# Performance work log

Hardware: AMD Instinct MI355X
Metric: run time of the kernel (lower is better)

The kernel has to match this reference:

```python
import jax, jax.numpy as jnp
import numpy as np

N = 100000
E = 1600000
IN_DIM = 128
OUT_DIM = 128
H = 4
HD = OUT_DIM // H  # 32
NEG_SLOPE = 0.2
EPS_SOFTMAX = 1e-8
EPS_LN = 1e-5


def setup_inputs() -> dict:
    key = jax.random.key(0)
    ks = jax.random.split(key, 6)
    h = jax.random.normal(ks[0], (N, IN_DIM), dtype=jnp.float32)
    edge_index = jax.random.randint(ks[1], (2, E), 0, N, dtype=jnp.int32)
    W = jax.random.normal(ks[2], (IN_DIM, OUT_DIM), dtype=jnp.float32) / np.sqrt(IN_DIM)
    W_self = jax.random.normal(ks[3], (IN_DIM, OUT_DIM), dtype=jnp.float32) / np.sqrt(IN_DIM)
    a_in = jax.random.normal(ks[4], (H, 2 * HD), dtype=jnp.float32) * 0.01
    a_out = jax.random.normal(ks[5], (H, 2 * HD), dtype=jnp.float32) * 0.01
    bias = jnp.zeros((OUT_DIM,), dtype=jnp.float32)
    ln_gamma = jnp.ones((OUT_DIM,), dtype=jnp.float32)
    ln_beta = jnp.zeros((OUT_DIM,), dtype=jnp.float32)
    return {"h": h, "edge_index": edge_index, "W": W, "W_self": W_self,
            "a_in": a_in, "a_out": a_out, "bias": bias,
            "ln_gamma": ln_gamma, "ln_beta": ln_beta}


def _attention_aggregate(h_proj, sender, receiver, attn_vec, num_nodes):
    # h_proj: (N, H, HD); sender/receiver: (E,); attn_vec: (H, 2*HD)
    h_sender = h_proj[sender]      # (E, H, HD)
    h_receiver = h_proj[receiver]  # (E, H, HD)
    # e = sum over concat([h_sender, h_receiver]) * attn_vec, split halves
    e = (jnp.einsum('ehd,hd->eh', h_sender, attn_vec[:, :HD])
         + jnp.einsum('ehd,hd->eh', h_receiver, attn_vec[:, HD:]))
    e = jax.nn.leaky_relu(e, NEG_SLOPE)
    e_max = jax.ops.segment_max(e, receiver, num_segments=num_nodes)  # (N, H)
    alpha = jnp.exp(e - e_max[receiver])
    alpha_sum = jax.ops.segment_sum(alpha, receiver, num_segments=num_nodes)
    alpha = alpha / (alpha_sum[receiver] + EPS_SOFTMAX)
    msg = h_sender * alpha[..., None]  # (E, H, HD)
    return jax.ops.segment_sum(msg, receiver, num_segments=num_nodes)  # (N, H, HD)


def reference(h, edge_index, W, W_self, a_in, a_out, bias, ln_gamma, ln_beta):
    n = h.shape[0]
    h_proj = (h @ W).reshape(n, H, HD)
    h_self = h @ W_self
    src, dst = edge_index[0], edge_index[1]
    h_in = _attention_aggregate(h_proj, src, dst, a_in, n)   # 'in' direction
    h_out = _attention_aggregate(h_proj, dst, src, a_out, n)  # 'out' direction
    combined = h_self + h_in.reshape(n, -1) + h_out.reshape(n, -1) + bias
    mean = combined.mean(axis=-1, keepdims=True)
    var = combined.var(axis=-1, keepdims=True)
    normed = (combined - mean) * jax.lax.rsqrt(var + EPS_LN)
    return normed * ln_gamma + ln_beta
```

## Files before the change

kernel.cpp:

```cpp
#include <hip/hip_runtime.h>
#include <math.h>

#define HEADS 4
#define HD 32
#define DIM 128
#define NEG_SLOPE 0.2f
#define EPS_SM 1e-8f
#define EPS_LN 1e-5f
#define GROWS 64
#define SH1 9
#define PB 128

typedef _Float16 h2_t __attribute__((ext_vector_type(2)));

__device__ __forceinline__ float lrelu(float x) { return x > 0.f ? x : NEG_SLOPE * x; }
__device__ __forceinline__ unsigned pkh(float a, float b) {
    return __builtin_bit_cast(unsigned, __builtin_amdgcn_cvt_pkrtz(a, b));
}
__device__ __forceinline__ float dot2(unsigned a, unsigned b, float c) {
    return __builtin_amdgcn_fdot2(__builtin_bit_cast(h2_t, a), __builtin_bit_cast(h2_t, b), c, false);
}

template<int LIM> __device__ __forceinline__ void rmax4(float& a, float& b, float& c, float& d) {
#pragma unroll
    for (int s = 1; s < LIM; s <<= 1) {
        a = fmaxf(a, __shfl_xor(a, s, 64));
        b = fmaxf(b, __shfl_xor(b, s, 64));
        c = fmaxf(c, __shfl_xor(c, s, 64));
        d = fmaxf(d, __shfl_xor(d, s, 64));
    }
}
template<int LIM> __device__ __forceinline__ void rsum4(float& a, float& b, float& c, float& d) {
#pragma unroll
    for (int s = 1; s < LIM; s <<= 1) {
        a += __shfl_xor(a, s, 64);
        b += __shfl_xor(b, s, 64);
        c += __shfl_xor(c, s, 64);
        d += __shfl_xor(d, s, 64);
    }
}

__global__ __launch_bounds__(256) void dual_gemm_k(const float* __restrict__ h,
                                                   const float* __restrict__ W,
                                                   const float* __restrict__ V,
                                                   const float* __restrict__ a_in,
                                                   const float* __restrict__ a_out,
                                                   float* __restrict__ h_self,
                                                   unsigned* __restrict__ hp_pk,
                                                   float* __restrict__ pA0, float* __restrict__ pA1,
                                                   float* __restrict__ pB0, float* __restrict__ pB1,
                                                   int N) {
    __shared__ float As[32][GROWS];
    __shared__ float Ws[32][DIM];
    __shared__ float Vs[32][DIM];
    __shared__ float ainL[256], aoutL[256];
    const int tid = threadIdx.x;
    const int cg = tid & 15;
    const int rg = tid >> 4;
    const int row0 = blockIdx.x * GROWS;

    ainL[tid] = a_in[tid];
    aoutL[tid] = a_out[tid];

    float accP[4][8], accS[4][8];
#pragma unroll
    for (int r = 0; r < 4; ++r)
#pragma unroll
        for (int c = 0; c < 8; ++c) { accP[r][c] = 0.f; accS[r][c] = 0.f; }

    for (int kc = 0; kc < 4; ++kc) {
        __syncthreads();
#pragma unroll
        for (int p = 0; p < 2; ++p) {
            int f = tid + p * 256;
            int r = f >> 3, c4 = f & 7;
            float4 v = make_float4(0.f, 0.f, 0.f, 0.f);
            if (row0 + r < N) v = ((const float4*)h)[(size_t)(row0 + r) * 32 + kc * 8 + c4];
            As[c4 * 4 + 0][r] = v.x;
            As[c4 * 4 + 1][r] = v.y;
            As[c4 * 4 + 2][r] = v.z;
            As[c4 * 4 + 3][r] = v.w;
        }
#pragma unroll
        for (int p = 0; p < 4; ++p) {
            int f = tid + p * 256;
            int lk = f >> 5, c4 = f & 31;
            ((float4*)&Ws[lk][0])[c4] = ((const float4*)W)[(size_t)(kc * 32 + lk) * 32 + c4];
            ((float4*)&Vs[lk][0])[c4] = ((const float4*)V)[(size_t)(kc * 32 + lk) * 32 + c4];
        }
        __syncthreads();
#pragma unroll
        for (int kk = 0; kk < 32; ++kk) {
            float4 a = *(const float4*)&As[kk][rg * 4];
            float4 w0 = *(const float4*)&Ws[kk][cg * 8];
            float4 w1 = *(const float4*)&Ws[kk][cg * 8 + 4];
            float4 v0 = *(const float4*)&Vs[kk][cg * 8];
            float4 v1 = *(const float4*)&Vs[kk][cg * 8 + 4];
            float av[4] = {a.x, a.y, a.z, a.w};
            float wv[8] = {w0.x, w0.y, w0.z, w0.w, w1.x, w1.y, w1.z, w1.w};
            float vv[8] = {v0.x, v0.y, v0.z, v0.w, v1.x, v1.y, v1.z, v1.w};
#pragma unroll
            for (int r = 0; r < 4; ++r)
#pragma unroll
                for (int c = 0; c < 8; ++c) {
                    accP[r][c] += av[r] * wv[c];
                    accS[r][c] += av[r] * vv[c];
                }
        }
    }

#pragma unroll
    for (int r = 0; r < 4; ++r) {
        int row = row0 + rg * 4 + r;
        if (row < N) {
            float4 s0 = make_float4(accS[r][0], accS[r][1], accS[r][2], accS[r][3]);
            float4 s1 = make_float4(accS[r][4], accS[r][5], accS[r][6], accS[r][7]);
            ((float4*)h_self)[(size_t)row * 32 + cg * 2] = s0;
            ((float4*)h_self)[(size_t)row * 32 + cg * 2 + 1] = s1;
        }
    }

    const int head = cg >> 2, qi = cg & 3;
#pragma unroll
    for (int r = 0; r < 4; ++r) {
        float d0 = 0.f, d1 = 0.f, d2 = 0.f, d3 = 0.f;
#pragma unroll
        for (int c = 0; c < 8; ++c) {
            float v = accP[r][c];
            int k = head * 64 + qi * 8 + c;
            d0 += v * ainL[k];
            d1 += v * ainL[k + 32];
            d2 += v * aoutL[k];
            d3 += v * aoutL[k + 32];
        }
        d0 += __shfl_xor(d0, 1, 64); d0 += __shfl_xor(d0, 2, 64);
        d1 += __shfl_xor(d1, 1, 64); d1 += __shfl_xor(d1, 2, 64);
        d2 += __shfl_xor(d2, 1, 64); d2 += __shfl_xor(d2, 2, 64);
        d3 += __shfl_xor(d3, 1, 64); d3 += __shfl_xor(d3, 2, 64);
        if (qi == 0) {
            int row = row0 + rg * 4 + r;
            if (row < N) {
                pA0[row * 4 + head] = d0;
                pA1[row * 4 + head] = d1;
                pB0[row * 4 + head] = d2;
                pB1[row * 4 + head] = d3;
            }
        }
    }

#pragma unroll
    for (int r = 0; r < 4; ++r) {
        int row = row0 + rg * 4 + r;
        if (row < N) {
            uint4 pk;
            pk.x = pkh(accP[r][0], accP[r][1]);
            pk.y = pkh(accP[r][2], accP[r][3]);
            pk.z = pkh(accP[r][4], accP[r][5]);
            pk.w = pkh(accP[r][6], accP[r][7]);
            ((uint4*)hp_pk)[(size_t)row * 16 + cg] = pk;
        }
    }
}

__global__ __launch_bounds__(256) void part1a_k(const int* __restrict__ ei, int* __restrict__ cntmat,
                                                int E, int N, int NBIN) {
    __shared__ int lcnt[512];
    const int t = threadIdx.x;
    const int CH = (E + gridDim.x - 1) / gridDim.x;
    const int e0 = blockIdx.x * CH;
    const int e1 = min(e0 + CH, E);
    for (int i = t; i < 512; i += 256) lcnt[i] = 0;
    __syncthreads();
    for (int e = e0 + t; e < e1; e += 256) {
        int s = ei[e], d = ei[E + e];
        atomicAdd(&lcnt[d >> SH1], 1);
        atomicAdd(&lcnt[(N + s) >> SH1], 1);
    }
    __syncthreads();
    for (int i = t; i < NBIN; i += 256) cntmat[i * PB + blockIdx.x] = lcnt[i];
}

__global__ __launch_bounds__(128) void scanB_k(const int* __restrict__ cntmat,
                                               int* __restrict__ blkoff, int* __restrict__ btot) {
    __shared__ int ls[PB];
    const int bin = blockIdx.x;
    const int t = threadIdx.x;
    int v = cntmat[bin * PB + t];
    ls[t] = v;
    __syncthreads();
#pragma unroll
    for (int d = 1; d < PB; d <<= 1) {
        int u = (t >= d) ? ls[t - d] : 0;
        __syncthreads();
        ls[t] += u;
        __syncthreads();
    }
    blkoff[bin * PB + t] = ls[t] - v;
    if (t == PB - 1) btot[bin] = ls[t];
}

__global__ __launch_bounds__(256) void scanC_k(const int* __restrict__ btot,
                                               int* __restrict__ bbase, int NBIN, int twoE) {
    __shared__ int ls[256];
    int t = threadIdx.x;
    int i0 = 2 * t, i1 = 2 * t + 1;
    int v0 = (i0 < NBIN) ? btot[i0] : 0;
    int v1 = (i1 < NBIN) ? btot[i1] : 0;
    int pair = v0 + v1;
    ls[t] = pair;
    __syncthreads();
#pragma unroll
    for (int d = 1; d < 256; d <<= 1) {
        int u = (t >= d) ? ls[t - d] : 0;
        __syncthreads();
        ls[t] += u;
        __syncthreads();
    }
    int excl = ls[t] - pair;
    if (i0 < NBIN) bbase[i0] = excl;
    if (i1 < NBIN) bbase[i1] = excl + v0;
    if (t == 0) bbase[NBIN] = twoE;
}

__global__ __launch_bounds__(256) void part1b_k(const int* __restrict__ ei,
                                                const int* __restrict__ bbase,
                                                const int* __restrict__ blkoff,
                                                unsigned* __restrict__ rec, int E, int N, int NBIN) {
    __shared__ int gb[512];
    __shared__ int lcur[512];
    const int t = threadIdx.x;
    const int CH = (E + gridDim.x - 1) / gridDim.x;
    const int e0 = blockIdx.x * CH;
    const int e1 = min(e0 + CH, E);
    for (int i = t; i < 512; i += 256) lcur[i] = 0;
    for (int i = t; i < NBIN; i += 256) gb[i] = bbase[i] + blkoff[i * PB + blockIdx.x];
    __syncthreads();
    for (int e = e0 + t; e < e1; e += 256) {
        int s = ei[e], d = ei[E + e];
        int b1 = d >> SH1;
        int r1 = atomicAdd(&lcur[b1], 1);
        rec[gb[b1] + r1] = (unsigned)s | ((unsigned)(d & 511) << 20);
        int so = N + s;
        int b2 = so >> SH1;
        int r2 = atomicAdd(&lcur[b2], 1);
        rec[gb[b2] + r2] = (unsigned)d | ((unsigned)(so & 511) << 20);
    }
}

__global__ __launch_bounds__(256) void build2_k(const unsigned* __restrict__ rec,
                                                const int* __restrict__ bbase,
                                                int* __restrict__ off, int* __restrict__ csr,
                                                int M, int twoE, int NBIN) {
    __shared__ int lcnt[512];
    __shared__ int lcur[512];
    __shared__ int ls[256];
    const int b = blockIdx.x;
    const int t = threadIdx.x;
    const int base = bbase[b];
    const int cnt = bbase[b + 1] - base;
    const int seg0 = b << SH1;
    for (int i = t; i < 512; i += 256) lcnt[i] = 0;
    __syncthreads();
    for (int k = t; k < cnt; k += 256) atomicAdd(&lcnt[rec[base + k] >> 20], 1);
    __syncthreads();
    int v0 = lcnt[2 * t], v1 = lcnt[2 * t + 1];
    int pair = v0 + v1;
    ls[t] = pair;
    __syncthreads();
#pragma unroll
    for (int d = 1; d < 256; d <<= 1) {
        int u = (t >= d) ? ls[t - d] : 0;
        __syncthreads();
        ls[t] += u;
        __syncthreads();
    }
    int excl = ls[t] - pair;
    lcur[2 * t] = excl;
    lcur[2 * t + 1] = excl + v0;
    int sg = seg0 + 2 * t;
    if (sg < M) off[sg] = base + excl;
    if (sg + 1 < M) off[sg + 1] = base + excl + v0;
    if (b == NBIN - 1 && t == 0) off[M] = twoE;
    __syncthreads();
    for (int k = t; k < cnt; k += 256) {
        unsigned r = rec[base + k];
        int pos = atomicAdd(&lcur[r >> 20], 1);
        csr[base + pos] = (int)(r & 0xFFFFFu);
    }
}

__global__ __launch_bounds__(256) void node_aggr_ln_k(const unsigned* __restrict__ hp_pk,
                                                      const float* __restrict__ h_self,
                                                      const float* __restrict__ pA0, const float* __restrict__ pA1,
                                                      const float* __restrict__ pB0, const float* __restrict__ pB1,
                                                      const int* __restrict__ off, const int* __restrict__ csr,
                                                      const float* __restrict__ bias,
                                                      const float* __restrict__ gamma,
                                                      const float* __restrict__ beta,
                                                      float* __restrict__ out, int N) {
    __shared__ int sds[4][64];
    __shared__ uint2 wts[4][64];
    const int wave = threadIdx.x >> 6;
    const int lane = threadIdx.x & 63;
    const int n = blockIdx.x * 4 + wave;
    if (n >= N) return;
    const int l15 = lane & 15;
    const int q = lane >> 4;
    const unsigned wsel = (l15 & 4) ? 0x07060302u : 0x05040100u;
    const bool hlo = (l15 < 8);
    int* sdw = sds[wave];
    uint2* wtw = wts[wave];
    const char* hpb = (const char*)hp_pk;
    const unsigned rowoff = (unsigned)l15 << 4;

    float acc[8];
#pragma unroll
    for (int k = 0; k < 8; ++k) acc[k] = 0.f;

#pragma unroll
    for (int dir = 0; dir < 2; ++dir) {
        const int seg = (dir == 0) ? n : N + n;
        const int beg = off[seg], end = off[seg + 1];
        const int len = end - beg;
        if (len == 0) continue;
        const float* __restrict__ p0 = (dir == 0) ? pA0 : pB0;
        const float* __restrict__ p1 = (dir == 0) ? pA1 : pB1;
        float4 r1 = ((const float4*)p1)[n];

        if (len <= 64) {
            int sid = 0;
            float e0 = -INFINITY, e1 = -INFINITY, e2 = -INFINITY, e3 = -INFINITY;
            if (lane < len) {
                sid = csr[beg + lane];
                float4 r0 = ((const float4*)p0)[sid];
                e0 = lrelu(r0.x + r1.x);
                e1 = lrelu(r0.y + r1.y);
                e2 = lrelu(r0.z + r1.z);
                e3 = lrelu(r0.w + r1.w);
            }
            float m0 = e0, m1 = e1, m2 = e2, m3 = e3;
            if (len <= 16)      rmax4<16>(m0, m1, m2, m3);
            else if (len <= 32) rmax4<32>(m0, m1, m2, m3);
            else                rmax4<64>(m0, m1, m2, m3);
            float w0 = 0.f, w1 = 0.f, w2 = 0.f, w3 = 0.f;
            if (lane < len) {
                w0 = __expf(e0 - m0); w1 = __expf(e1 - m1);
                w2 = __expf(e2 - m2); w3 = __expf(e3 - m3);
            }
            float s0 = w0, s1 = w1, s2 = w2, s3 = w3;
            if (len <= 16)      rsum4<16>(s0, s1, s2, s3);
            else if (len <= 32) rsum4<32>(s0, s1, s2, s3);
            else                rsum4<64>(s0, s1, s2, s3);
            w0 *= 1.f / (s0 + EPS_SM);
            w1 *= 1.f / (s1 + EPS_SM);
            w2 *= 1.f / (s2 + EPS_SM);
            w3 *= 1.f / (s3 + EPS_SM);
            sdw[lane] = sid;
            wtw[lane] = make_uint2(pkh(w0, w1), pkh(w2, w3));
            const int npair = (len + 7) >> 3;
#pragma unroll 2
            for (int t = 0; t < npair; ++t) {
                int pi = 4 * t + q;
                uint2 sp = *(const uint2*)&sdw[2 * pi];
                uint4 wp = *(const uint4*)&wtw[2 * pi];
                uint4 u = *(const uint4*)(hpb + (((unsigned)sp.x << 8) + rowoff));
                uint4 v = *(const uint4*)(hpb + (((unsigned)sp.y << 8) + rowoff));
                unsigned wA = hlo ? wp.x : wp.y;
                unsigned wB = hlo ? wp.z : wp.w;
                unsigned wpk = __builtin_amdgcn_perm(wB, wA, wsel);
                acc[0] = dot2(__builtin_amdgcn_perm(v.x, u.x, 0x05040100u), wpk, acc[0]);
                acc[1] = dot2(__builtin_amdgcn_perm(v.x, u.x, 0x07060302u), wpk, acc[1]);
                acc[2] = dot2(__builtin_amdgcn_perm(v.y, u.y, 0x05040100u), wpk, acc[2]);
                acc[3] = dot2(__builtin_amdgcn_perm(v.y, u.y, 0x07060302u), wpk, acc[3]);
                acc[4] = dot2(__builtin_amdgcn_perm(v.z, u.z, 0x05040100u), wpk, acc[4]);
                acc[5] = dot2(__builtin_amdgcn_perm(v.z, u.z, 0x07060302u), wpk, acc[5]);
                acc[6] = dot2(__builtin_amdgcn_perm(v.w, u.w, 0x05040100u), wpk, acc[6]);
                acc[7] = dot2(__builtin_amdgcn_perm(v.w, u.w, 0x07060302u), wpk, acc[7]);
            }
        } else {
            float m0 = -INFINITY, m1 = -INFINITY, m2 = -INFINITY, m3 = -INFINITY;
            for (int base = beg; base < end; base += 64) {
                int j = base + lane;
                if (j < end) {
                    int sid = csr[j];
                    float4 r0 = ((const float4*)p0)[sid];
                    m0 = fmaxf(m0, lrelu(r0.x + r1.x));
                    m1 = fmaxf(m1, lrelu(r0.y + r1.y));
                    m2 = fmaxf(m2, lrelu(r0.z + r1.z));
                    m3 = fmaxf(m3, lrelu(r0.w + r1.w));
                }
            }
            rmax4<64>(m0, m1, m2, m3);
            float s0 = 0.f, s1 = 0.f, s2 = 0.f, s3 = 0.f;
            for (int base = beg; base < end; base += 64) {
                int j = base + lane;
                if (j < end) {
                    int sid = csr[j];
                    float4 r0 = ((const float4*)p0)[sid];
                    s0 += __expf(lrelu(r0.x + r1.x) - m0);
                    s1 += __expf(lrelu(r0.y + r1.y) - m1);
                    s2 += __expf(lrelu(r0.z + r1.z) - m2);
                    s3 += __expf(lrelu(r0.w + r1.w) - m3);
                }
            }
            rsum4<64>(s0, s1, s2, s3);
            const float is0 = 1.f / (s0 + EPS_SM);
            const float is1 = 1.f / (s1 + EPS_SM);
            const float is2 = 1.f / (s2 + EPS_SM);
            const float is3 = 1.f / (s3 + EPS_SM);
            for (int base = beg; base < end; base += 64) {
                int cnt = min(64, end - base);
                int sid = 0;
                float w0 = 0.f, w1 = 0.f, w2 = 0.f, w3 = 0.f;
                if (lane < cnt) {
                    sid = csr[base + lane];
                    float4 r0 = ((const float4*)p0)[sid];
                    w0 = __expf(lrelu(r0.x + r1.x) - m0) * is0;
                    w1 = __expf(lrelu(r0.y + r1.y) - m1) * is1;
                    w2 = __expf(lrelu(r0.z + r1.z) - m2) * is2;
                    w3 = __expf(lrelu(r0.w + r1.w) - m3) * is3;
                }
                sdw[lane] = sid;
                wtw[lane] = make_uint2(pkh(w0, w1), pkh(w2, w3));
                const int npair = (cnt + 7) >> 3;
#pragma unroll 2
                for (int t = 0; t < npair; ++t) {
                    int pi = 4 * t + q;
                    uint2 sp = *(const uint2*)&sdw[2 * pi];
                    uint4 wp = *(const uint4*)&wtw[2 * pi];
                    uint4 u = *(const uint4*)(hpb + (((unsigned)sp.x << 8) + rowoff));
                    uint4 v = *(const uint4*)(hpb + (((unsigned)sp.y << 8) + rowoff));
                    unsigned wA = hlo ? wp.x : wp.y;
                    unsigned wB = hlo ? wp.z : wp.w;
                    unsigned wpk = __builtin_amdgcn_perm(wB, wA, wsel);
                    acc[0] = dot2(__builtin_amdgcn_perm(v.x, u.x, 0x05040100u), wpk, acc[0]);
                    acc[1] = dot2(__builtin_amdgcn_perm(v.x, u.x, 0x07060302u), wpk, acc[1]);
                    acc[2] = dot2(__builtin_amdgcn_perm(v.y, u.y, 0x05040100u), wpk, acc[2]);
                    acc[3] = dot2(__builtin_amdgcn_perm(v.y, u.y, 0x07060302u), wpk, acc[3]);
                    acc[4] = dot2(__builtin_amdgcn_perm(v.z, u.z, 0x05040100u), wpk, acc[4]);
                    acc[5] = dot2(__builtin_amdgcn_perm(v.z, u.z, 0x07060302u), wpk, acc[5]);
                    acc[6] = dot2(__builtin_amdgcn_perm(v.w, u.w, 0x05040100u), wpk, acc[6]);
                    acc[7] = dot2(__builtin_amdgcn_perm(v.w, u.w, 0x07060302u), wpk, acc[7]);
                }
            }
        }
    }

#pragma unroll
    for (int s = 16; s < 64; s <<= 1) {
#pragma unroll
        for (int k = 0; k < 8; ++k) acc[k] += __shfl_xor(acc[k], s, 64);
    }

    size_t bb = (size_t)n * DIM;
    float4 hs0 = ((const float4*)(h_self + bb))[2 * l15];
    float4 hs1 = ((const float4*)(h_self + bb))[2 * l15 + 1];
    float4 b0 = ((const float4*)bias)[2 * l15];
    float4 b1 = ((const float4*)bias)[2 * l15 + 1];
    float x0 = hs0.x + acc[0] + b0.x;
    float x1 = hs0.y + acc[1] + b0.y;
    float x2 = hs0.z + acc[2] + b0.z;
    float x3 = hs0.w + acc[3] + b0.w;
    float y0 = hs1.x + acc[4] + b1.x;
    float y1 = hs1.y + acc[5] + b1.y;
    float y2 = hs1.z + acc[6] + b1.z;
    float y3 = hs1.w + acc[7] + b1.w;
    float sum = x0 + x1 + x2 + x3 + y0 + y1 + y2 + y3;
    float sq = x0 * x0 + x1 * x1 + x2 * x2 + x3 * x3
             + y0 * y0 + y1 * y1 + y2 * y2 + y3 * y3;
#pragma unroll
    for (int m = 1; m < 64; m <<= 1) {
        sum += __shfl_xor(sum, m, 64);
        sq += __shfl_xor(sq, m, 64);
    }
    float mean = sum * (1.f / 512.f);
    float var = sq * (1.f / 512.f) - mean * mean;
    float inv = rsqrtf(var + EPS_LN);
    if (lane < 16) {
        float4 g0 = ((const float4*)gamma)[2 * l15];
        float4 g1 = ((const float4*)gamma)[2 * l15 + 1];
        float4 be0 = ((const float4*)beta)[2 * l15];
        float4 be1 = ((const float4*)beta)[2 * l15 + 1];
        float4 o0 = make_float4((x0 - mean) * inv * g0.x + be0.x,
                                (x1 - mean) * inv * g0.y + be0.y,
                                (x2 - mean) * inv * g0.z + be0.z,
                                (x3 - mean) * inv * g0.w + be0.w);
        float4 o1 = make_float4((y0 - mean) * inv * g1.x + be1.x,
                                (y1 - mean) * inv * g1.y + be1.y,
                                (y2 - mean) * inv * g1.z + be1.z,
                                (y3 - mean) * inv * g1.w + be1.w);
        ((float4*)(out + bb))[2 * l15] = o0;
        ((float4*)(out + bb))[2 * l15 + 1] = o1;
    }
}

extern "C" void kernel_launch(void* const* d_in, const int* in_sizes, int n_in,
                              void* d_out, int out_size, void* d_ws, size_t ws_size,
                              hipStream_t stream) {
    const float* h      = (const float*)d_in[0];
    const int*   ei     = (const int*)d_in[1];
    const float* W      = (const float*)d_in[2];
    const float* W_self = (const float*)d_in[3];
    const float* a_in   = (const float*)d_in[4];
    const float* a_out  = (const float*)d_in[5];
    const float* bias   = (const float*)d_in[6];
    const float* gamma  = (const float*)d_in[7];
    const float* beta   = (const float*)d_in[8];
    float* out = (float*)d_out;

    const int N = in_sizes[0] / DIM;
    const int E = in_sizes[1] / 2;
    const int M = 2 * N;
    const int NBIN = (M + (1 << SH1) - 1) >> SH1;
    const int twoE = 2 * E;

    float* ws = (float*)d_ws;
    size_t off_f = 0;
    float* h_self = ws + off_f; off_f += (size_t)N * DIM;
    unsigned* hp_pk = (unsigned*)(ws + off_f); off_f += (size_t)N * 64;
    float* pA0 = ws + off_f; off_f += (size_t)N * 4;
    float* pA1 = ws + off_f; off_f += (size_t)N * 4;
    float* pB0 = ws + off_f; off_f += (size_t)N * 4;
    float* pB1 = ws + off_f; off_f += (size_t)N * 4;
    int* ip = (int*)(ws + off_f);
    size_t off_i = 0;
    int* cntmat = ip + off_i; off_i += (size_t)NBIN * PB;
    int* blkoff = ip + off_i; off_i += (size_t)NBIN * PB;
    int* btot   = ip + off_i; off_i += NBIN;
    int* bbase  = ip + off_i; off_i += (size_t)NBIN + 1;
    int* off    = ip + off_i; off_i += (size_t)M + 1;
    unsigned* rec = (unsigned*)(ip + off_i); off_i += (size_t)twoE;
    int* csr    = ip + off_i; off_i += (size_t)twoE;

    part1a_k<<<PB, 256, 0, stream>>>(ei, cntmat, E, N, NBIN);
    scanB_k<<<NBIN, PB, 0, stream>>>(cntmat, blkoff, btot);
    scanC_k<<<1, 256, 0, stream>>>(btot, bbase, NBIN, twoE);
    part1b_k<<<PB, 256, 0, stream>>>(ei, bbase, blkoff, rec, E, N, NBIN);
    build2_k<<<NBIN, 256, 0, stream>>>(rec, bbase, off, csr, M, twoE, NBIN);

    dual_gemm_k<<<(N + GROWS - 1) / GROWS, 256, 0, stream>>>(h, W, W_self, a_in, a_out,
                                                             h_self, hp_pk, pA0, pA1, pB0, pB1, N);

    node_aggr_ln_k<<<(N + 3) / 4, 256, 0, stream>>>(hp_pk, h_self, pA0, pA1, pB0, pB1,
                                                    off, csr, bias, gamma, beta, out, N);
}
```

Measured before the change: 454.6 us.

## Replace FP32 dual GEMM with fp16 MFMA GEMM and folded attention columns

Replaces the scalar FP32 shared-memory GEMM with an MFMA 16x16x32 fp16 kernel. A small pre-kernel converts W, W_self and the attention vectors into one transposed fp16 B matrix, where 16 extra columns fold the per-head attention dot products (W·a) into the GEMM. This removes the FP32 FMA-bound projection and the separate shuffle reductions. In exchange, h and the weights are rounded to fp16 with fp32 accumulation, which lowers the precision of h_self and the attention logits, and B is read directly from global/L2 without LDS staging.

Result: faster. 417.1 us (-8.2%).

```diff
diff --git a/kernel.cpp b/kernel.cpp
--- a/kernel.cpp
+++ b/kernel.cpp
@@ -7,11 +7,13 @@
 #define NEG_SLOPE 0.2f
 #define EPS_SM 1e-8f
 #define EPS_LN 1e-5f
-#define GROWS 64
 #define SH1 9
 #define PB 128
+#define BCOLS 272
 
 typedef _Float16 h2_t __attribute__((ext_vector_type(2)));
+typedef _Float16 f16x8 __attribute__((ext_vector_type(8)));
+typedef float f32x4 __attribute__((ext_vector_type(4)));
 
 __device__ __forceinline__ float lrelu(float x) { return x > 0.f ? x : NEG_SLOPE * x; }
 __device__ __forceinline__ unsigned pkh(float a, float b) {
@@ -40,125 +42,98 @@
     }
 }
 
-__global__ __launch_bounds__(256) void dual_gemm_k(const float* __restrict__ h,
-                                                   const float* __restrict__ W,
-                                                   const float* __restrict__ V,
-                                                   const float* __restrict__ a_in,
-                                                   const float* __restrict__ a_out,
+__global__ __launch_bounds__(128) void cvtb_k(const float* __restrict__ W,
+                                              const float* __restrict__ V,
+                                              const float* __restrict__ a_in,
+                                              const float* __restrict__ a_out,
+                                              _Float16* __restrict__ Bt) {
+    const int c = blockIdx.x;
+    const int k = threadIdx.x;
+    float v;
+    if (c < 128) {
+        v = W[k * 128 + c];
+    } else if (c < 256) {
+        v = V[k * 128 + (c - 128)];
+    } else {
+        int d = (c - 256) >> 2, h = (c - 256) & 3;
+        const float* a = (d < 2) ? a_in : a_out;
+        int base = h * 64 + (d & 1) * 32;
+        float s = 0.f;
+#pragma unroll
+        for (int t = 0; t < 32; ++t) s += W[k * 128 + 32 * h + t] * a[base + t];
+        v = s;
+    }
+    Bt[c * 128 + k] = (_Float16)v;
+}
+
+__global__ __launch_bounds__(256) void mfma_gemm_k(const float* __restrict__ h,
+                                                   const _Float16* __restrict__ Bt,
                                                    float* __restrict__ h_self,
                                                    unsigned* __restrict__ hp_pk,
                                                    float* __restrict__ pA0, float* __restrict__ pA1,
                                                    float* __restrict__ pB0, float* __restrict__ pB1,
                                                    int N) {
-    __shared__ float As[32][GROWS];
-    __shared__ float Ws[32][DIM];
-    __shared__ float Vs[32][DIM];
-    __shared__ float ainL[256], aoutL[256];
+    __shared__ _Float16 hs[64][128];
     const int tid = threadIdx.x;
-    const int cg = tid & 15;
-    const int rg = tid >> 4;
-    const int row0 = blockIdx.x * GROWS;
-
-    ainL[tid] = a_in[tid];
-    aoutL[tid] = a_out[tid];
-
-    float accP[4][8], accS[4][8];
-#pragma unroll
-    for (int r = 0; r < 4; ++r)
-#pragma unroll
-        for (int c = 0; c < 8; ++c) { accP[r][c] = 0.f; accS[r][c] = 0.f; }
-
+    const int w = tid >> 6, l = tid & 63;
+    const int l15 = l & 15;
+    const int kg = l >> 4;
+    const int row0 = blockIdx.x * 64;
+    const int arow = row0 + 16 * w + l15;
+
+    f32x4 acc[17];
+#pragma unroll
+    for (int j = 0; j < 17; ++j) {
+        acc[j][0] = 0.f; acc[j][1] = 0.f; acc[j][2] = 0.f; acc[j][3] = 0.f;
+    }
+
+    const uint4* __restrict__ bt4 = (const uint4*)Bt;
+
+#pragma unroll
     for (int kc = 0; kc < 4; ++kc) {
-        __syncthreads();
-#pragma unroll
-        for (int p = 0; p < 2; ++p) {
-            int f = tid + p * 256;
-            int r = f >> 3, c4 = f & 7;
-            float4 v = make_float4(0.f, 0.f, 0.f, 0.f);
-            if (row0 + r < N) v = ((const float4*)h)[(size_t)(row0 + r) * 32 + kc * 8 + c4];
-            As[c4 * 4 + 0][r] = v.x;
-            As[c4 * 4 + 1][r] = v.y;
-            As[c4 * 4 + 2][r] = v.z;
-            As[c4 * 4 + 3][r] = v.w;
+        union { unsigned u[4]; f16x8 v; } cv;
+        if (arow < N) {
+            float4 x0 = ((const float4*)h)[(size_t)arow * 32 + kc * 8 + kg * 2];
+            float4 x1 = ((const float4*)h)[(size_t)arow * 32 + kc * 8 + kg * 2 + 1];
+            cv.u[0] = pkh(x0.x, x0.y); cv.u[1] = pkh(x0.z, x0.w);
+            cv.u[2] = pkh(x1.x, x1.y); cv.u[3] = pkh(x1.z, x1.w);
+        } else {
+            cv.u[0] = 0u; cv.u[1] = 0u; cv.u[2] = 0u; cv.u[3] = 0u;
         }
-#pragma unroll
-        for (int p = 0; p < 4; ++p) {
-            int f = tid + p * 256;
-            int lk = f >> 5, c4 = f & 31;
-            ((float4*)&Ws[lk][0])[c4] = ((const float4*)W)[(size_t)(kc * 32 + lk) * 32 + c4];
-            ((float4*)&Vs[lk][0])[c4] = ((const float4*)V)[(size_t)(kc * 32 + lk) * 32 + c4];
+        f16x8 af = cv.v;
+#pragma unroll
+        for (int j = 0; j < 17; ++j) {
+            int col = 16 * j + l15;
+            union { uint4 q; f16x8 v; } bc;
+            bc.q = bt4[col * 16 + kc * 4 + kg];
+            acc[j] = __builtin_amdgcn_mfma_f32_16x16x32_f16(af, bc.v, acc[j], 0, 0, 0);
         }
-        __syncthreads();
-#pragma unroll
-        for (int kk = 0; kk < 32; ++kk) {
-            float4 a = *(const float4*)&As[kk][rg * 4];
-            float4 w0 = *(const float4*)&Ws[kk][cg * 8];
-            float4 w1 = *(const float4*)&Ws[kk][cg * 8 + 4];
-            float4 v0 = *(const float4*)&Vs[kk][cg * 8];
-            float4 v1 = *(const float4*)&Vs[kk][cg * 8 + 4];
-            float av[4] = {a.x, a.y, a.z, a.w};
-            float wv[8] = {w0.x, w0.y, w0.z, w0.w, w1.x, w1.y, w1.z, w1.w};
-            float vv[8] = {v0.x, v0.y, v0.z, v0.w, v1.x, v1.y, v1.z, v1.w};
-#pragma unroll
-            for (int r = 0; r < 4; ++r)
-#pragma unroll
-                for (int c = 0; c < 8; ++c) {
-                    accP[r][c] += av[r] * wv[c];
-                    accS[r][c] += av[r] * vv[c];
-                }
-        }
-    }
-
+    }
+
+    const int r4 = kg * 4;
+    const int c16 = l15, dsel = c16 >> 2, hh = c16 & 3;
+    float* __restrict__ pd = (dsel == 0) ? pA0 : (dsel == 1) ? pA1 : (dsel == 2) ? pB0 : pB1;
 #pragma unroll
     for (int r = 0; r < 4; ++r) {
-        int row = row0 + rg * 4 + r;
-        if (row < N) {
-            float4 s0 = make_float4(accS[r][0], accS[r][1], accS[r][2], accS[r][3]);
-            float4 s1 = make_float4(accS[r][4], accS[r][5], accS[r][6], accS[r][7]);
-            ((float4*)h_self)[(size_t)row * 32 + cg * 2] = s0;
-            ((float4*)h_self)[(size_t)row * 32 + cg * 2 + 1] = s1;
-        }
-    }
-
-    const int head = cg >> 2, qi = cg & 3;
-#pragma unroll
-    for (int r = 0; r < 4; ++r) {
-        float d0 = 0.f, d1 = 0.f, d2 = 0.f, d3 = 0.f;
-#pragma unroll
-        for (int c = 0; c < 8; ++c) {
-            float v = accP[r][c];
-            int k = head * 64 + qi * 8 + c;
-            d0 += v * ainL[k];
-            d1 += v * ainL[k + 32];
-            d2 += v * aoutL[k];
-            d3 += v * aoutL[k + 32];
-        }
-        d0 += __shfl_xor(d0, 1, 64); d0 += __shfl_xor(d0, 2, 64);
-        d1 += __shfl_xor(d1, 1, 64); d1 += __shfl_xor(d1, 2, 64);
-        d2 += __shfl_xor(d2, 1, 64); d2 += __shfl_xor(d2, 2, 64);
-        d3 += __shfl_xor(d3, 1, 64); d3 += __shfl_xor(d3, 2, 64);
-        if (qi == 0) {
-            int row = row0 + rg * 4 + r;
-            if (row < N) {
-                pA0[row * 4 + head] = d0;
-                pA1[row * 4 + head] = d1;
-                pB0[row * 4 + head] = d2;
-                pB1[row * 4 + head] = d3;
-            }
-        }
-    }
-
-#pragma unroll
-    for (int r = 0; r < 4; ++r) {
-        int row = row0 + rg * 4 + r;
-        if (row < N) {
-            uint4 pk;
-            pk.x = pkh(accP[r][0], accP[r][1]);
-            pk.y = pkh(accP[r][2], accP[r][3]);
-            pk.z = pkh(accP[r][4], accP[r][5]);
-            pk.w = pkh(accP[r][6], accP[r][7]);
-            ((uint4*)hp_pk)[(size_t)row * 16 + cg] = pk;
-        }
+        int grow = row0 + 16 * w + r4 + r;
+        bool ok = grow < N;
+#pragma unroll
+        for (int j = 8; j < 16; ++j)
+            if (ok) h_self[(size_t)grow * 128 + 16 * (j - 8) + l15] = acc[j][r];
+        if (ok) pd[grow * 4 + hh] = acc[16][r];
+#pragma unroll
+        for (int j = 0; j < 8; ++j)
+            hs[16 * w + r4 + r][16 * j + l15] = (_Float16)acc[j][r];
+    }
+    __syncthreads();
+    const uint4* hsv = (const uint4*)&hs[0][0];
+#pragma unroll
+    for (int p = 0; p < 4; ++p) {
+        int chunk = tid + p * 256;
+        int rrow = chunk >> 4, cg = chunk & 15;
+        int grow = row0 + rrow;
+        if (grow < N)
+            ((uint4*)hp_pk)[(size_t)grow * 16 + cg] = hsv[rrow * 16 + cg];
     }
 }
 
@@ -531,6 +506,9 @@
     int* off    = ip + off_i; off_i += (size_t)M + 1;
     unsigned* rec = (unsigned*)(ip + off_i); off_i += (size_t)twoE;
     int* csr    = ip + off_i; off_i += (size_t)twoE;
+    _Float16* Bt = (_Float16*)(ip + off_i); off_i += (size_t)(BCOLS * 128) / 2;
+
+    cvtb_k<<<BCOLS, 128, 0, stream>>>(W, W_self, a_in, a_out, Bt);
 
     part1a_k<<<PB, 256, 0, stream>>>(ei, cntmat, E, N, NBIN);
     scanB_k<<<NBIN, PB, 0, stream>>>(cntmat, blkoff, btot);
@@ -538,8 +516,8 @@
     part1b_k<<<PB, 256, 0, stream>>>(ei, bbase, blkoff, rec, E, N, NBIN);
     build2_k<<<NBIN, 256, 0, stream>>>(rec, bbase, off, csr, M, twoE, NBIN);
 
-    dual_gemm_k<<<(N + GROWS - 1) / GROWS, 256, 0, stream>>>(h, W, W_self, a_in, a_out,
-                                                             h_self, hp_pk, pA0, pA1, pB0, pB1, N);
+    mfma_gemm_k<<<(N + 63) / 64, 256, 0, stream>>>(h, Bt, h_self, hp_pk,
+                                                   pA0, pA1, pB0, pB1, N);
 
     node_aggr_ln_k<<<(N + 3) / 4, 256, 0, stream>>>(hp_pk, h_self, pA0, pA1, pB0, pB1,
                                                     off, csr, bias, gamma, beta, out, N);
```
